# Performance work log

Hardware: AMD Instinct MI355X
Metric: run time of the kernel (lower is better)

## Reference

```python
import jax, jax.numpy as jnp
import numpy as np

N = 100000   # nodes
E = 1600000  # edges
F = 128      # num_features
H = 128      # embedding_size
C = 10       # num_classes
G = 64       # graphs in batch


def setup_inputs() -> dict:
    key = jax.random.key(0)
    ks = jax.random.split(key, 10)
    x = jax.random.normal(ks[0], (N, F), jnp.float32)
    edge_index = jax.random.randint(ks[1], (2, E), 0, N)
    batch_index = jnp.sort(jax.random.randint(ks[2], (N,), 0, G))
    glorot = lambda k, shape: jax.random.normal(k, shape, jnp.float32) / np.float32(np.sqrt(shape[0]))
    return {
        "x": x, "edge_index": edge_index, "batch_index": batch_index,
        "W0": glorot(ks[3], (F, H)), "b0": jnp.zeros((H,), jnp.float32),
        "W1": glorot(ks[4], (H, H)), "b1": jnp.zeros((H,), jnp.float32),
        "W2": glorot(ks[5], (H, H)), "b2": jnp.zeros((H,), jnp.float32),
        "W3": glorot(ks[6], (H, H)), "b3": jnp.zeros((H,), jnp.float32),
        "Wout": glorot(ks[7], (2 * H, C)), "bout": jnp.zeros((C,), jnp.float32),
    }


def gcn_conv(x, W, b, src, dst):
    """PyG GCNConv: self-loops + symmetric D^-1/2 (A+I) D^-1/2 normalization."""
    n = x.shape[0]
    # degree with self-loop: deg[i] = 1 + in-degree(i)
    deg = 1.0 + jax.ops.segment_sum(jnp.ones(dst.shape[0], x.dtype), dst, num_segments=n)
    dinv = jax.lax.rsqrt(deg)
    h = x @ W  # [N, H]
    norm = (dinv[src] * dinv[dst])[:, None]  # [E, 1]
    agg = jax.ops.segment_sum(h[src] * norm, dst, num_segments=n)  # scatter-add over edges
    agg = agg + h * (1.0 / deg)[:, None]  # self-loop contribution dinv[i]^2 * h[i]
    return agg + b


def reference(x, edge_index, batch_index, W0, b0, W1, b1, W2, b2, W3, b3, Wout, bout):
    src, dst = edge_index[0], edge_index[1]
    h = jnp.tanh(gcn_conv(x, W0, b0, src, dst))
    h = jnp.tanh(gcn_conv(h, W1, b1, src, dst))
    h = jnp.tanh(gcn_conv(h, W2, b2, src, dst))
    h = jnp.tanh(gcn_conv(h, W3, b3, src, dst))
    # global max pool + global mean pool over batch_index
    gmax = jax.ops.segment_max(h, batch_index, num_segments=G)
    cnt = jax.ops.segment_sum(jnp.ones((h.shape[0],), h.dtype), batch_index, num_segments=G)
    gmean = jax.ops.segment_sum(h, batch_index, num_segments=G) / jnp.maximum(cnt, 1.0)[:, None]
    pooled = jnp.concatenate([gmax, gmean], axis=1)  # [G, 2H]
    out = pooled @ Wout + bout  # [G, C]
    return out, pooled
```

## Files before the change

kernel.cpp:

```cpp
#include <hip/hip_runtime.h>
#include <hip/hip_fp16.h>
#include <cmath>

typedef __attribute__((ext_vector_type(8))) short short8;
typedef __attribute__((ext_vector_type(8))) unsigned short ushort8;
typedef __attribute__((ext_vector_type(4))) float f32x4;

struct h8 { __half2 a, b, c, d; };


__global__ __launch_bounds__(256) void count_k(const int* __restrict__ dst,
                                               int* __restrict__ cnt,
                                               int* __restrict__ epos, int E) {
  int e = blockIdx.x * 256 + threadIdx.x;
  if (e < E) epos[e] = atomicAdd(&cnt[dst[e]], 1);
}

__global__ __launch_bounds__(256) void dinv_k(const int* __restrict__ cnt,
                                              float* __restrict__ dinv,
                                              float* __restrict__ dinv2, int N) {
  int i = blockIdx.x * 256 + threadIdx.x;
  if (i < N) {
    float deg = 1.0f + (float)cnt[i];
    dinv[i] = rsqrtf(deg);
    dinv2[i] = 1.0f / deg;
  }
}

__global__ __launch_bounds__(512) void scan_a(const int* __restrict__ cnt,
                                              int* __restrict__ rs,
                                              int* __restrict__ bsum, int n) {
  __shared__ int s[512];
  int tid = threadIdx.x;
  int gid = blockIdx.x * 512 + tid;
  int v = (gid < n) ? cnt[gid] : 0;
  s[tid] = v;
  __syncthreads();
  for (int off = 1; off < 512; off <<= 1) {
    int t = (tid >= off) ? s[tid - off] : 0;
    __syncthreads();
    s[tid] += t;
    __syncthreads();
  }
  if (gid < n) rs[gid] = s[tid] - v;
  if (tid == 511) bsum[blockIdx.x] = s[511];
}

__global__ __launch_bounds__(256) void scan_b(const int* __restrict__ bsum,
                                              int* __restrict__ boff, int nb) {
  __shared__ int s[256];
  int tid = threadIdx.x;
  int v = (tid < nb) ? bsum[tid] : 0;
  s[tid] = v;
  __syncthreads();
  for (int off = 1; off < 256; off <<= 1) {
    int t = (tid >= off) ? s[tid - off] : 0;
    __syncthreads();
    s[tid] += t;
    __syncthreads();
  }
  if (tid < nb) boff[tid] = s[tid] - v;
}

__global__ __launch_bounds__(512) void scan_c(const int* __restrict__ boff,
                                              int* __restrict__ rs, int n, int E) {
  int gid = blockIdx.x * 512 + threadIdx.x;
  if (gid < n) rs[gid] += boff[blockIdx.x];
  if (gid == 0) rs[n] = E;
}

__global__ __launch_bounds__(256) void fill_k(const int* __restrict__ src,
                                              const int* __restrict__ dst,
                                              const int* __restrict__ rs,
                                              const int* __restrict__ epos,
                                              const float* __restrict__ dinv,
                                              int* __restrict__ col,
                                              float* __restrict__ normv, int E) {
  int e = blockIdx.x * 256 + threadIdx.x;
  if (e >= E) return;
  int s = src[e], d = dst[e];
  int pos = rs[d] + epos[e];
  col[pos] = s;
  normv[pos] = dinv[s] * dinv[d];
}


__global__ __launch_bounds__(256) void wconv_all(const float* __restrict__ W0,
                                                 const float* __restrict__ W1,
                                                 const float* __restrict__ W2,
                                                 const float* __restrict__ W3,
                                                 unsigned short* __restrict__ WtHi,
                                                 unsigned short* __restrict__ WtLo) {
  int l = blockIdx.y;
  const float* W = (l == 0) ? W0 : (l == 1) ? W1 : (l == 2) ? W2 : W3;
  int t = blockIdx.x * 256 + threadIdx.x;
  if (t >= 16384) return;
  int k = t >> 7, n = t & 127;
  float w = W[t];
  unsigned int u = __float_as_uint(w);
  unsigned short hb = (unsigned short)((u + 0x7FFFu + ((u >> 16) & 1u)) >> 16);
  float hf = __uint_as_float(((unsigned int)hb) << 16);
  float lf = w - hf;
  unsigned int ul = __float_as_uint(lf);
  unsigned short lb = (unsigned short)((ul + 0x7FFFu + ((ul >> 16) & 1u)) >> 16);
  WtHi[l * 16384 + n * 128 + k] = hb;
  WtLo[l * 16384 + n * 128 + k] = lb;
}


#define LDK 136

__global__ __launch_bounds__(256) void gemm_mfma(const float* __restrict__ A,
                                                 const unsigned short* __restrict__ WtHi,
                                                 const unsigned short* __restrict__ WtLo,
                                                 __half* __restrict__ O, int M) {
  __shared__ unsigned short sHi[128 * LDK];
  __shared__ unsigned short sLo[128 * LDK];
  int tid = threadIdx.x;
#pragma unroll
  for (int i = 0; i < 8; ++i) {
    int c = tid + i * 256;
    int n = c >> 4;
    int off = (c & 15) * 8;
    *(ushort8*)&sHi[n * LDK + off] = *(const ushort8*)&WtHi[c * 8];
    *(ushort8*)&sLo[n * LDK + off] = *(const ushort8*)&WtLo[c * 8];
  }
  __syncthreads();

  int wv = tid >> 6, lane = tid & 63;
  int r0 = blockIdx.x * 128 + wv * 32;
  int lrow = lane & 15, lk = (lane >> 4) * 8;

  f32x4 acc[2][8] = {};
#pragma unroll
  for (int kk = 0; kk < 4; ++kk) {
    int k0 = kk * 32 + lk;
    short8 ahi[2], alo[2];
#pragma unroll
    for (int fr = 0; fr < 2; ++fr) {
      int row = r0 + fr * 16 + lrow;
      row = row < M ? row : M - 1;
      const float* ap = &A[(size_t)row * 128 + k0];
      float4 a0 = *(const float4*)ap;
      float4 a1 = *(const float4*)(ap + 4);
      float av[8] = {a0.x, a0.y, a0.z, a0.w, a1.x, a1.y, a1.z, a1.w};
      union { short8 v; unsigned short u[8]; } h_, l_;
#pragma unroll
      for (int j = 0; j < 8; ++j) {
        unsigned int u = __float_as_uint(av[j]);
        unsigned short hb = (unsigned short)((u + 0x7FFFu + ((u >> 16) & 1u)) >> 16);
        float hf = __uint_as_float(((unsigned int)hb) << 16);
        float lf = av[j] - hf;
        unsigned int ul = __float_as_uint(lf);
        h_.u[j] = hb;
        l_.u[j] = (unsigned short)((ul + 0x7FFFu + ((ul >> 16) & 1u)) >> 16);
      }
      ahi[fr] = h_.v;
      alo[fr] = l_.v;
    }
#pragma unroll
    for (int c = 0; c < 8; ++c) {
      int bidx = (c * 16 + lrow) * LDK + k0;
      short8 bhi = *(const short8*)&sHi[bidx];
      short8 blo = *(const short8*)&sLo[bidx];
#pragma unroll
      for (int fr = 0; fr < 2; ++fr) {
        acc[fr][c] = __builtin_amdgcn_mfma_f32_16x16x32_bf16(ahi[fr], bhi, acc[fr][c], 0, 0, 0);
        acc[fr][c] = __builtin_amdgcn_mfma_f32_16x16x32_bf16(ahi[fr], blo, acc[fr][c], 0, 0, 0);
        acc[fr][c] = __builtin_amdgcn_mfma_f32_16x16x32_bf16(alo[fr], bhi, acc[fr][c], 0, 0, 0);
      }
    }
  }
#pragma unroll
  for (int fr = 0; fr < 2; ++fr) {
#pragma unroll
    for (int c = 0; c < 8; ++c) {
#pragma unroll
      for (int r = 0; r < 4; ++r) {
        int row = r0 + fr * 16 + (lane >> 4) * 4 + r;
        if (row < M)
          O[(size_t)row * 128 + c * 16 + (lane & 15)] = __float2half(acc[fr][c][r]);
      }
    }
  }
}


__global__ __launch_bounds__(256) void gather_k(const __half* __restrict__ h,
                                                const int* __restrict__ rs,
                                                const int* __restrict__ col,
                                                const float* __restrict__ normv,
                                                const float* __restrict__ dinv2,
                                                const float* __restrict__ bias,
                                                float* __restrict__ out, int N) {
  int wid = (int)((blockIdx.x * (size_t)blockDim.x + threadIdx.x) >> 6);
  if (wid >= N) return;
  int lane = threadIdx.x & 63;
  int grp = lane >> 4;
  int li = lane & 15;
  int s = rs[wid], e = rs[wid + 1];
  const h8* hrow = (const h8*)h;

  float ac[8] = {};
  int n16 = (e - s) >> 4;
  int base = s + grp;
  for (int it = 0; it < n16; ++it, base += 16) {
    int c0 = col[base], c1 = col[base + 4], c2 = col[base + 8], c3 = col[base + 12];
    float w0 = normv[base], w1 = normv[base + 4], w2 = normv[base + 8],
          w3 = normv[base + 12];
    h8 v0 = hrow[(size_t)c0 * 16 + li];
    h8 v1 = hrow[(size_t)c1 * 16 + li];
    h8 v2 = hrow[(size_t)c2 * 16 + li];
    h8 v3 = hrow[(size_t)c3 * 16 + li];
#define ACC(V, W)                                    \
    {                                                \
      float2 f0 = __half22float2((V).a);             \
      float2 f1 = __half22float2((V).b);             \
      float2 f2 = __half22float2((V).c);             \
      float2 f3 = __half22float2((V).d);             \
      ac[0] += (W) * f0.x; ac[1] += (W) * f0.y;      \
      ac[2] += (W) * f1.x; ac[3] += (W) * f1.y;      \
      ac[4] += (W) * f2.x; ac[5] += (W) * f2.y;      \
      ac[6] += (W) * f3.x; ac[7] += (W) * f3.y;      \
    }
    ACC(v0, w0) ACC(v1, w1) ACC(v2, w2) ACC(v3, w3)
  }
  for (int idx = base; idx < e; idx += 4) {
    int c = col[idx];
    float w = normv[idx];
    h8 v = hrow[(size_t)c * 16 + li];
    ACC(v, w)
  }
#undef ACC
#pragma unroll
  for (int j = 0; j < 8; ++j) {
    ac[j] += __shfl_xor(ac[j], 16);
    ac[j] += __shfl_xor(ac[j], 32);
  }

  float d2 = dinv2[wid];
  h8 sv = hrow[(size_t)wid * 16 + li];
  float2 s0 = __half22float2(sv.a), s1 = __half22float2(sv.b),
         s2 = __half22float2(sv.c), s3 = __half22float2(sv.d);
  float svf[8] = {s0.x, s0.y, s1.x, s1.y, s2.x, s2.y, s3.x, s3.y};
  float4 b0 = ((const float4*)bias)[li * 2];
  float4 b1 = ((const float4*)bias)[li * 2 + 1];
  float bvf[8] = {b0.x, b0.y, b0.z, b0.w, b1.x, b1.y, b1.z, b1.w};
  float o[8];
#pragma unroll
  for (int j = 0; j < 8; ++j) o[j] = tanhf(ac[j] + svf[j] * d2 + bvf[j]);
  if (grp == 0) {
    float4* op = (float4*)&out[(size_t)wid * 128 + li * 8];
    op[0] = make_float4(o[0], o[1], o[2], o[3]);
    op[1] = make_float4(o[4], o[5], o[6], o[7]);
  }
}


__global__ __launch_bounds__(128) void bounds_k(const int* __restrict__ batch,
                                                int* __restrict__ gstart, int n,
                                                int G) {
  int t = threadIdx.x;
  if (t > G) return;
  int lo = 0, hi = n;
  while (lo < hi) {
    int mid = (lo + hi) >> 1;
    if (batch[mid] < t) lo = mid + 1;
    else hi = mid;
  }
  gstart[t] = lo;
}

#define CH 16

__global__ __launch_bounds__(128) void pool_partial(const float* __restrict__ h,
                                                    const int* __restrict__ gstart,
                                                    float* __restrict__ pmax,
                                                    float* __restrict__ psum) {
  int g = blockIdx.x, c = blockIdx.y, f = threadIdx.x;
  int s = gstart[g], e = gstart[g + 1];
  long long len = e - s;
  int cs = s + (int)(len * c / CH);
  int ce = s + (int)(len * (c + 1) / CH);
  float m = -INFINITY, sum = 0.f;
  for (int n = cs; n < ce; ++n) {
    float v = h[(size_t)n * 128 + f];
    m = fmaxf(m, v);
    sum += v;
  }
  pmax[((size_t)g * CH + c) * 128 + f] = m;
  psum[((size_t)g * CH + c) * 128 + f] = sum;
}

__global__ __launch_bounds__(128) void pool_final(const float* __restrict__ pmax,
                                                  const float* __restrict__ psum,
                                                  const int* __restrict__ gstart,
                                                  float* __restrict__ pooled) {
  int g = blockIdx.x, f = threadIdx.x;
  float m = -INFINITY, s = 0.f;
  for (int c = 0; c < CH; ++c) {
    m = fmaxf(m, pmax[((size_t)g * CH + c) * 128 + f]);
    s += psum[((size_t)g * CH + c) * 128 + f];
  }
  int cnt = gstart[g + 1] - gstart[g];
  float mean = s / fmaxf((float)cnt, 1.0f);
  pooled[(size_t)g * 256 + f] = m;
  pooled[(size_t)g * 256 + 128 + f] = mean;
}

__global__ __launch_bounds__(64) void out_mm(const float* __restrict__ pooled,
                                             const float* __restrict__ Wout,
                                             const float* __restrict__ bout,
                                             float* __restrict__ out) {
  __shared__ float p[256];
  int g = blockIdx.x, t = threadIdx.x;
  for (int i = t; i < 256; i += 64) p[i] = pooled[(size_t)g * 256 + i];
  __syncthreads();
  if (t < 10) {
    float acc = bout[t];
    for (int k = 0; k < 256; ++k) acc += p[k] * Wout[k * 10 + t];
    out[(size_t)g * 10 + t] = acc;
  }
}


extern "C" void kernel_launch(void* const* d_in, const int* in_sizes, int n_in,
                              void* d_out, int out_size, void* d_ws, size_t ws_size,
                              hipStream_t stream) {
  const float* x = (const float*)d_in[0];
  const int* ei = (const int*)d_in[1];
  const int* batch = (const int*)d_in[2];
  const float* W[4] = {(const float*)d_in[3], (const float*)d_in[5],
                       (const float*)d_in[7], (const float*)d_in[9]};
  const float* Bz[4] = {(const float*)d_in[4], (const float*)d_in[6],
                        (const float*)d_in[8], (const float*)d_in[10]};
  const float* Wout = (const float*)d_in[11];
  const float* bout = (const float*)d_in[12];
  const int N = in_sizes[0] / 128;
  const int E = in_sizes[1] / 2;
  const int G = 64;
  const int* srcp = ei;
  const int* dstp = ei + E;
  float* out = (float*)d_out;

  char* wsb = (char*)d_ws;
  size_t off = 0;
  auto alloc = [&](size_t bytes) -> void* {
    void* p = wsb + off;
    off = (off + bytes + 255) & ~(size_t)255;
    return p;
  };
  __half* bufA = (__half*)alloc((size_t)N * 128 * 2);
  float* bufB = (float*)alloc((size_t)N * 128 * 4);
  int* cnt = (int*)alloc((size_t)N * 4);
  int* epos = (int*)alloc((size_t)E * 4);
  float* dinv = (float*)alloc((size_t)N * 4);
  float* dinv2 = (float*)alloc((size_t)N * 4);
  int* rs = (int*)alloc((size_t)(N + 1) * 4);
  int* col = (int*)alloc((size_t)E * 4);
  float* normv = (float*)alloc((size_t)E * 4);
  int* bsum = (int*)alloc(4096);
  int* boff = (int*)alloc(4096);
  int* gstart = (int*)alloc(4096);
  float* pmax = (float*)alloc((size_t)G * CH * 128 * 4);
  float* psum = (float*)alloc((size_t)G * CH * 128 * 4);
  unsigned short* WtHi = (unsigned short*)alloc(4 * 16384 * 2);
  unsigned short* WtLo = (unsigned short*)alloc(4 * 16384 * 2);
  if (off > ws_size) return;

  hipMemsetAsync(cnt, 0, (size_t)N * 4, stream);

  count_k<<<(E + 255) / 256, 256, 0, stream>>>(dstp, cnt, epos, E);
  dinv_k<<<(N + 255) / 256, 256, 0, stream>>>(cnt, dinv, dinv2, N);
  int nsb = (N + 511) / 512;
  scan_a<<<nsb, 512, 0, stream>>>(cnt, rs, bsum, N);
  scan_b<<<1, 256, 0, stream>>>(bsum, boff, nsb);
  scan_c<<<nsb, 512, 0, stream>>>(boff, rs, N, E);
  fill_k<<<(E + 255) / 256, 256, 0, stream>>>(srcp, dstp, rs, epos, dinv, col,
                                              normv, E);
  bounds_k<<<1, 128, 0, stream>>>(batch, gstart, N, G);
  wconv_all<<<dim3(64, 4), 256, 0, stream>>>(W[0], W[1], W[2], W[3], WtHi, WtLo);

  const float* in = x;
  for (int l = 0; l < 4; ++l) {
    gemm_mfma<<<(N + 127) / 128, 256, 0, stream>>>(in, WtHi + l * 16384,
                                                   WtLo + l * 16384, bufA, N);
    gather_k<<<((size_t)N * 64 + 255) / 256, 256, 0, stream>>>(bufA, rs, col, normv,
                                                               dinv2, Bz[l], bufB, N);
    in = bufB;
  }

  pool_partial<<<dim3(G, CH), 128, 0, stream>>>(bufB, gstart, pmax, psum);
  pool_final<<<G, 128, 0, stream>>>(pmax, psum, gstart, out + G * 10);
  out_mm<<<G, 64, 0, stream>>>(out + G * 10, Wout, bout, out);
}
```

Measured before the change: 547.8 us.

## Fuse small kernels, use packed bf16 conversion and fast tanh epilogue

Folds dinv computation into scan_a, graph-boundary search into scan_b, and pool_final plus the output matmul into one pool_head kernel, which removes several launches. Replaces the manual bf16 round-and-split with the packed v_cvt_pk_bf16_f32 instruction in both the weight conversion and the GEMM A-operand split. The gather epilogue now has each lane group handle two features with an exp/rcp tanh instead of computing all eight and keeping one group's result. Fast tanh and rcp slightly reduce accuracy, and the split-precision GEMM now depends on the hardware conversion's rounding.

```diff
diff --git a/kernel.cpp b/kernel.cpp
--- a/kernel.cpp
+++ b/kernel.cpp
@@ -7,6 +7,17 @@
 typedef __attribute__((ext_vector_type(4))) float f32x4;
 
 struct h8 { __half2 a, b, c, d; };
+
+__device__ __forceinline__ unsigned pk_bf16(float a, float b) {
+  unsigned r;
+  asm("v_cvt_pk_bf16_f32 %0, %1, %2" : "=v"(r) : "v"(a), "v"(b));
+  return r;
+}
+
+__device__ __forceinline__ float fast_tanh(float x) {
+  float e2 = __expf(2.0f * x);
+  return 1.0f - 2.0f * __builtin_amdgcn_rcpf(e2 + 1.0f);
+}
 
 
 __global__ __launch_bounds__(256) void count_k(const int* __restrict__ dst,
@@ -16,24 +27,20 @@
   if (e < E) epos[e] = atomicAdd(&cnt[dst[e]], 1);
 }
 
-__global__ __launch_bounds__(256) void dinv_k(const int* __restrict__ cnt,
-                                              float* __restrict__ dinv,
-                                              float* __restrict__ dinv2, int N) {
-  int i = blockIdx.x * 256 + threadIdx.x;
-  if (i < N) {
-    float deg = 1.0f + (float)cnt[i];
-    dinv[i] = rsqrtf(deg);
-    dinv2[i] = 1.0f / deg;
-  }
-}
-
 __global__ __launch_bounds__(512) void scan_a(const int* __restrict__ cnt,
                                               int* __restrict__ rs,
-                                              int* __restrict__ bsum, int n) {
+                                              int* __restrict__ bsum,
+                                              float* __restrict__ dinv,
+                                              float* __restrict__ dinv2, int n) {
   __shared__ int s[512];
   int tid = threadIdx.x;
   int gid = blockIdx.x * 512 + tid;
   int v = (gid < n) ? cnt[gid] : 0;
+  if (gid < n) {
+    float deg = 1.0f + (float)v;
+    dinv[gid] = rsqrtf(deg);
+    dinv2[gid] = __builtin_amdgcn_rcpf(deg);
+  }
   s[tid] = v;
   __syncthreads();
   for (int off = 1; off < 512; off <<= 1) {
@@ -47,7 +54,10 @@
 }
 
 __global__ __launch_bounds__(256) void scan_b(const int* __restrict__ bsum,
-                                              int* __restrict__ boff, int nb) {
+                                              int* __restrict__ boff, int nb,
+                                              const int* __restrict__ batch,
+                                              int* __restrict__ gstart, int n,
+                                              int G) {
   __shared__ int s[256];
   int tid = threadIdx.x;
   int v = (tid < nb) ? bsum[tid] : 0;
@@ -60,6 +70,15 @@
     __syncthreads();
   }
   if (tid < nb) boff[tid] = s[tid] - v;
+  if (tid <= G) {
+    int lo = 0, hi = n;
+    while (lo < hi) {
+      int mid = (lo + hi) >> 1;
+      if (batch[mid] < tid) lo = mid + 1;
+      else hi = mid;
+    }
+    gstart[tid] = lo;
+  }
 }
 
 __global__ __launch_bounds__(512) void scan_c(const int* __restrict__ boff,
@@ -93,18 +112,16 @@
                                                  unsigned short* __restrict__ WtLo) {
   int l = blockIdx.y;
   const float* W = (l == 0) ? W0 : (l == 1) ? W1 : (l == 2) ? W2 : W3;
-  int t = blockIdx.x * 256 + threadIdx.x;
-  if (t >= 16384) return;
-  int k = t >> 7, n = t & 127;
-  float w = W[t];
-  unsigned int u = __float_as_uint(w);
-  unsigned short hb = (unsigned short)((u + 0x7FFFu + ((u >> 16) & 1u)) >> 16);
-  float hf = __uint_as_float(((unsigned int)hb) << 16);
-  float lf = w - hf;
-  unsigned int ul = __float_as_uint(lf);
-  unsigned short lb = (unsigned short)((ul + 0x7FFFu + ((ul >> 16) & 1u)) >> 16);
-  WtHi[l * 16384 + n * 128 + k] = hb;
-  WtLo[l * 16384 + n * 128 + k] = lb;
+  int idx = blockIdx.x * 256 + threadIdx.x;
+  if (idx >= 8192) return;
+  int n = idx & 127, k = (idx >> 7) * 2;
+  float w0 = W[k * 128 + n], w1 = W[(k + 1) * 128 + n];
+  unsigned h01 = pk_bf16(w0, w1);
+  float hf0 = __uint_as_float(h01 << 16);
+  float hf1 = __uint_as_float(h01 & 0xFFFF0000u);
+  unsigned l01 = pk_bf16(w0 - hf0, w1 - hf1);
+  *(unsigned*)&WtHi[l * 16384 + n * 128 + k] = h01;
+  *(unsigned*)&WtLo[l * 16384 + n * 128 + k] = l01;
 }
 
 
@@ -143,18 +160,20 @@
       const float* ap = &A[(size_t)row * 128 + k0];
       float4 a0 = *(const float4*)ap;
       float4 a1 = *(const float4*)(ap + 4);
-      float av[8] = {a0.x, a0.y, a0.z, a0.w, a1.x, a1.y, a1.z, a1.w};
-      union { short8 v; unsigned short u[8]; } h_, l_;
-#pragma unroll
-      for (int j = 0; j < 8; ++j) {
-        unsigned int u = __float_as_uint(av[j]);
-        unsigned short hb = (unsigned short)((u + 0x7FFFu + ((u >> 16) & 1u)) >> 16);
-        float hf = __uint_as_float(((unsigned int)hb) << 16);
-        float lf = av[j] - hf;
-        unsigned int ul = __float_as_uint(lf);
-        h_.u[j] = hb;
-        l_.u[j] = (unsigned short)((ul + 0x7FFFu + ((ul >> 16) & 1u)) >> 16);
+      union { short8 v; unsigned u32[4]; } h_, l_;
+#define SPLIT2(slot, x, y)                              \
+      {                                                 \
+        unsigned hh = pk_bf16((x), (y));                \
+        h_.u32[slot] = hh;                              \
+        float hf0 = __uint_as_float(hh << 16);          \
+        float hf1 = __uint_as_float(hh & 0xFFFF0000u);  \
+        l_.u32[slot] = pk_bf16((x) - hf0, (y) - hf1);   \
       }
+      SPLIT2(0, a0.x, a0.y)
+      SPLIT2(1, a0.z, a0.w)
+      SPLIT2(2, a1.x, a1.y)
+      SPLIT2(3, a1.z, a1.w)
+#undef SPLIT2
       ahi[fr] = h_.v;
       alo[fr] = l_.v;
     }
@@ -238,38 +257,19 @@
     ac[j] += __shfl_xor(ac[j], 32);
   }
 
+  float a0 = grp == 0 ? ac[0] : grp == 1 ? ac[2] : grp == 2 ? ac[4] : ac[6];
+  float a1 = grp == 0 ? ac[1] : grp == 1 ? ac[3] : grp == 2 ? ac[5] : ac[7];
+
   float d2 = dinv2[wid];
   h8 sv = hrow[(size_t)wid * 16 + li];
-  float2 s0 = __half22float2(sv.a), s1 = __half22float2(sv.b),
-         s2 = __half22float2(sv.c), s3 = __half22float2(sv.d);
-  float svf[8] = {s0.x, s0.y, s1.x, s1.y, s2.x, s2.y, s3.x, s3.y};
-  float4 b0 = ((const float4*)bias)[li * 2];
-  float4 b1 = ((const float4*)bias)[li * 2 + 1];
-  float bvf[8] = {b0.x, b0.y, b0.z, b0.w, b1.x, b1.y, b1.z, b1.w};
-  float o[8];
-#pragma unroll
-  for (int j = 0; j < 8; ++j) o[j] = tanhf(ac[j] + svf[j] * d2 + bvf[j]);
-  if (grp == 0) {
-    float4* op = (float4*)&out[(size_t)wid * 128 + li * 8];
-    op[0] = make_float4(o[0], o[1], o[2], o[3]);
-    op[1] = make_float4(o[4], o[5], o[6], o[7]);
-  }
-}
-
-
-__global__ __launch_bounds__(128) void bounds_k(const int* __restrict__ batch,
-                                                int* __restrict__ gstart, int n,
-                                                int G) {
-  int t = threadIdx.x;
-  if (t > G) return;
-  int lo = 0, hi = n;
-  while (lo < hi) {
-    int mid = (lo + hi) >> 1;
-    if (batch[mid] < t) lo = mid + 1;
-    else hi = mid;
-  }
-  gstart[t] = lo;
-}
+  __half2 svh = grp == 0 ? sv.a : grp == 1 ? sv.b : grp == 2 ? sv.c : sv.d;
+  float2 sj = __half22float2(svh);
+  float2 bj = *(const float2*)&bias[li * 8 + 2 * grp];
+  float o0 = fast_tanh(a0 + sj.x * d2 + bj.x);
+  float o1 = fast_tanh(a1 + sj.y * d2 + bj.y);
+  *(float2*)&out[(size_t)wid * 128 + li * 8 + 2 * grp] = make_float2(o0, o1);
+}
+
 
 #define CH 16
 
@@ -292,10 +292,13 @@
   psum[((size_t)g * CH + c) * 128 + f] = sum;
 }
 
-__global__ __launch_bounds__(128) void pool_final(const float* __restrict__ pmax,
-                                                  const float* __restrict__ psum,
-                                                  const int* __restrict__ gstart,
-                                                  float* __restrict__ pooled) {
+__global__ __launch_bounds__(128) void pool_head(const float* __restrict__ pmax,
+                                                 const float* __restrict__ psum,
+                                                 const int* __restrict__ gstart,
+                                                 const float* __restrict__ Wout,
+                                                 const float* __restrict__ bout,
+                                                 float* __restrict__ out, int G) {
+  __shared__ float pl[256];
   int g = blockIdx.x, f = threadIdx.x;
   float m = -INFINITY, s = 0.f;
   for (int c = 0; c < CH; ++c) {
@@ -304,22 +307,16 @@
   }
   int cnt = gstart[g + 1] - gstart[g];
   float mean = s / fmaxf((float)cnt, 1.0f);
+  float* pooled = out + (size_t)G * 10;
   pooled[(size_t)g * 256 + f] = m;
   pooled[(size_t)g * 256 + 128 + f] = mean;
-}
-
-__global__ __launch_bounds__(64) void out_mm(const float* __restrict__ pooled,
-                                             const float* __restrict__ Wout,
-                                             const float* __restrict__ bout,
-                                             float* __restrict__ out) {
-  __shared__ float p[256];
-  int g = blockIdx.x, t = threadIdx.x;
-  for (int i = t; i < 256; i += 64) p[i] = pooled[(size_t)g * 256 + i];
+  pl[f] = m;
+  pl[128 + f] = mean;
   __syncthreads();
-  if (t < 10) {
-    float acc = bout[t];
-    for (int k = 0; k < 256; ++k) acc += p[k] * Wout[k * 10 + t];
-    out[(size_t)g * 10 + t] = acc;
+  if (f < 10) {
+    float acc = bout[f];
+    for (int k = 0; k < 256; ++k) acc += pl[k] * Wout[k * 10 + f];
+    out[(size_t)g * 10 + f] = acc;
   }
 }
 
@@ -371,15 +368,13 @@
   hipMemsetAsync(cnt, 0, (size_t)N * 4, stream);
 
   count_k<<<(E + 255) / 256, 256, 0, stream>>>(dstp, cnt, epos, E);
-  dinv_k<<<(N + 255) / 256, 256, 0, stream>>>(cnt, dinv, dinv2, N);
   int nsb = (N + 511) / 512;
-  scan_a<<<nsb, 512, 0, stream>>>(cnt, rs, bsum, N);
-  scan_b<<<1, 256, 0, stream>>>(bsum, boff, nsb);
+  scan_a<<<nsb, 512, 0, stream>>>(cnt, rs, bsum, dinv, dinv2, N);
+  scan_b<<<1, 256, 0, stream>>>(bsum, boff, nsb, batch, gstart, N, G);
   scan_c<<<nsb, 512, 0, stream>>>(boff, rs, N, E);
   fill_k<<<(E + 255) / 256, 256, 0, stream>>>(srcp, dstp, rs, epos, dinv, col,
                                               normv, E);
-  bounds_k<<<1, 128, 0, stream>>>(batch, gstart, N, G);
-  wconv_all<<<dim3(64, 4), 256, 0, stream>>>(W[0], W[1], W[2], W[3], WtHi, WtLo);
+  wconv_all<<<dim3(32, 4), 256, 0, stream>>>(W[0], W[1], W[2], W[3], WtHi, WtLo);
 
   const float* in = x;
   for (int l = 0; l < 4; ++l) {
@@ -391,6 +386,5 @@
   }
 
   pool_partial<<<dim3(G, CH), 128, 0, stream>>>(bufB, gstart, pmax, psum);
-  pool_final<<<G, 128, 0, stream>>>(pmax, psum, gstart, out + G * 10);
-  out_mm<<<G, 64, 0, stream>>>(out + G * 10, Wout, bout, out);
-}
+  pool_head<<<G, 128, 0, stream>>>(pmax, psum, gstart, Wout, bout, out, G);
+}
```

Measured after the change: 541.3 us. About the same (-1.2%).
